# Kernel optimization log

Measured on AMD Instinct MI355X. Metric: run time of the kernel, lower is better.

Reference implementation:

```python
import jax, jax.numpy as jnp
import numpy as np

F, N, D, K = 32, 4096, 64, 512
COMMITMENT_COST = 0.25


def setup_inputs() -> dict:
    key = jax.random.key(0)
    k1, k2 = jax.random.split(key)
    inputs = jax.random.normal(k1, (F, N, D), dtype=jnp.float32)
    # GlorotUniform on weight shape [F, D, K]
    limit = float(np.sqrt(6.0 / (D + K)))
    w = jax.random.uniform(k2, (F, D, K), dtype=jnp.float32, minval=-limit, maxval=limit)
    return {"inputs": inputs, "w": w}


def reference(inputs, w):
    # inputs: [F, N, D], w: [F, D, K]
    distances = (
        jnp.sum(inputs ** 2, axis=2, keepdims=True)
        - 2.0 * jnp.einsum('fnd,fdk->fnk', inputs, w)
        + jnp.sum(w ** 2, axis=1, keepdims=True)
    )
    enc_idx = jnp.argmin(distances, axis=2)  # [F, N]
    w_t = jnp.swapaxes(w, 1, 2)  # [F, K, D]
    quantized = jnp.take_along_axis(w_t, enc_idx[:, :, None], axis=1)  # [F, N, D]
    e_latent_loss = jnp.mean((jax.lax.stop_gradient(quantized) - inputs) ** 2)
    q_latent_loss = jnp.mean((quantized - jax.lax.stop_gradient(inputs)) ** 2)
    loss = q_latent_loss + COMMITMENT_COST * e_latent_loss
    # straight-through estimator
    output = inputs + jax.lax.stop_gradient(quantized - inputs)
    return output, loss
```

## Files before the change

kernel.cpp:

```cpp
#include <hip/hip_runtime.h>
#include <math.h>

#define NF 32
#define NN 4096
#define ND 64
#define NK 512

#define LOSS_SCALE (1.25f / (float)(NF * NN * ND))
#define TAU 3e-4f

#define NPARTIAL (NF * NN * 4 / 256)

typedef short bf16x8 __attribute__((ext_vector_type(8)));
typedef float f32x4 __attribute__((ext_vector_type(4)));

static __device__ __forceinline__ unsigned short f2bf_rne(float f) {
    unsigned int u = __float_as_uint(f);
    u += 0x7FFFu + ((u >> 16) & 1u);
    return (unsigned short)(u >> 16);
}
static __device__ __forceinline__ float bf2f(unsigned short h) {
    return __uint_as_float(((unsigned int)h) << 16);
}

static __device__ __forceinline__ void gload_lds16(const void* g, void* l) {
    __builtin_amdgcn_global_load_lds(
        (const __attribute__((address_space(1))) unsigned int*)g,
        (__attribute__((address_space(3))) unsigned int*)l, 16, 0, 0);
}

__global__ __launch_bounds__(256)
void vq_prep_w(const float* __restrict__ w, float* __restrict__ wt,
               unsigned short* __restrict__ wh, unsigned short* __restrict__ wl,
               float* __restrict__ w2h) {
    const int gid = blockIdx.x * 256 + threadIdx.x;
    const int dc = gid & 7;
    const int k  = (gid >> 3) & (NK - 1);
    const int f  = gid >> 12;
    const float* __restrict__ wf = w + (size_t)f * ND * NK;
    const size_t rowo = ((size_t)f * NK + k) * ND + dc * 8;

    float v[8];
    unsigned short hh[8], ll[8];
    float s = 0.0f;
#pragma unroll
    for (int j = 0; j < 8; ++j) {
        v[j] = wf[(dc * 8 + j) * NK + k];
        s = fmaf(v[j], v[j], s);
        hh[j] = f2bf_rne(v[j]);
        ll[j] = f2bf_rne(v[j] - bf2f(hh[j]));
    }
    *(float4*)(wt + rowo)     = make_float4(v[0], v[1], v[2], v[3]);
    *(float4*)(wt + rowo + 4) = make_float4(v[4], v[5], v[6], v[7]);
    *(ushort4*)(wh + rowo)     = make_ushort4(hh[0], hh[1], hh[2], hh[3]);
    *(ushort4*)(wh + rowo + 4) = make_ushort4(hh[4], hh[5], hh[6], hh[7]);
    *(ushort4*)(wl + rowo)     = make_ushort4(ll[0], ll[1], ll[2], ll[3]);
    *(ushort4*)(wl + rowo + 4) = make_ushort4(ll[4], ll[5], ll[6], ll[7]);

    s += __shfl_xor(s, 1, 64);
    s += __shfl_xor(s, 2, 64);
    s += __shfl_xor(s, 4, 64);
    if (dc == 0) w2h[f * NK + k] = 0.5f * s;
}

__global__ __launch_bounds__(256, 4)
void vq_argmin(const float* __restrict__ x_in,
               const unsigned short* __restrict__ wh,
               const unsigned short* __restrict__ wl,
               const float* __restrict__ w2h,
               float* __restrict__ pm1,
               float* __restrict__ pm2,
               float* __restrict__ pkm) {
    const int b2   = blockIdx.x;
    const int h    = b2 & 1;
    const int b    = b2 >> 1;
    const int j    = b >> 3;
    const int f    = (b & 7) * 4 + (j & 3);
    const int xt   = j >> 2;
    const int tid  = threadIdx.x;
    const int wave = tid >> 6;
    const int lane = tid & 63;
    const int lc   = lane & 15;
    const int q    = lane >> 4;
    const int n0   = xt * 128 + wave * 32;

    __shared__ float w2s[256];
    __shared__ __align__(16) unsigned short bstage[2][4096];

    w2s[tid] = w2h[f * NK + h * 256 + tid];

    bf16x8 ah[2][2], al[2][2];
    const float* __restrict__ xbase = x_in + ((size_t)f * NN + n0 + lc) * ND;
#pragma unroll
    for (int mt = 0; mt < 2; ++mt) {
#pragma unroll
        for (int s = 0; s < 2; ++s) {
            const float* p = xbase + mt * 16 * ND + s * 32 + q * 8;
            float4 u0 = *(const float4*)(p);
            float4 u1 = *(const float4*)(p + 4);
            float xv[8] = {-u0.x, -u0.y, -u0.z, -u0.w, -u1.x, -u1.y, -u1.z, -u1.w};
            bf16x8 hh, ll;
#pragma unroll
            for (int jj = 0; jj < 8; ++jj) {
                unsigned short hb = f2bf_rne(xv[jj]);
                unsigned short lb = f2bf_rne(xv[jj] - bf2f(hb));
                hh[jj] = (short)hb;
                ll[jj] = (short)lb;
            }
            ah[mt][s] = hh;
            al[mt][s] = ll;
        }
    }

    const unsigned short* __restrict__ whf = wh + (size_t)f * NK * ND;
    const unsigned short* __restrict__ wlf = wl + (size_t)f * NK * ND;

    float m1[8], m2[8], kmin[8];
#pragma unroll
    for (int ri = 0; ri < 8; ++ri) { m1[ri] = INFINITY; m2[ri] = INFINITY; kmin[ri] = INFINITY; }

#define STAGE(st, pb) do {                                                  \
    _Pragma("unroll")                                                       \
    for (int rep = 0; rep < 2; ++rep) {                                     \
        const int c  = wave * 2 + rep;                                      \
        const int tl = c >> 2;                                              \
        const int sg = (c >> 1) & 1;                                        \
        const unsigned short* src = ((c & 1) ? wlf : whf) +                 \
            (size_t)((h * 8 + (st)) * 32 + tl * 16 + lc) * ND + q * 8 + sg * 32; \
        gload_lds16(src, &bstage[pb][c * 512]);                             \
    }                                                                       \
} while (0)

    STAGE(0, 0);

    for (int st = 0; st < 8; ++st) {
        __syncthreads();
        if (st < 7) STAGE(st + 1, (st + 1) & 1);
        const unsigned short* __restrict__ bb = &bstage[st & 1][0];

#pragma unroll
        for (int tl = 0; tl < 2; ++tl) {
            const int col = h * 256 + st * 32 + tl * 16 + lc;
            bf16x8 bh0 = *(const bf16x8*)(bb + (tl * 4 + 0) * 512 + lane * 8);
            bf16x8 bl0 = *(const bf16x8*)(bb + (tl * 4 + 1) * 512 + lane * 8);
            bf16x8 bh1 = *(const bf16x8*)(bb + (tl * 4 + 2) * 512 + lane * 8);
            bf16x8 bl1 = *(const bf16x8*)(bb + (tl * 4 + 3) * 512 + lane * 8);
            const float w2 = w2s[st * 32 + tl * 16 + lc];
#pragma unroll
            for (int mt = 0; mt < 2; ++mt) {
                f32x4 c = {w2, w2, w2, w2};
                c = __builtin_amdgcn_mfma_f32_16x16x32_bf16(ah[mt][0], bh0, c, 0, 0, 0);
                c = __builtin_amdgcn_mfma_f32_16x16x32_bf16(ah[mt][1], bh1, c, 0, 0, 0);
                c = __builtin_amdgcn_mfma_f32_16x16x32_bf16(ah[mt][0], bl0, c, 0, 0, 0);
                c = __builtin_amdgcn_mfma_f32_16x16x32_bf16(ah[mt][1], bl1, c, 0, 0, 0);
                c = __builtin_amdgcn_mfma_f32_16x16x32_bf16(al[mt][0], bh0, c, 0, 0, 0);
                c = __builtin_amdgcn_mfma_f32_16x16x32_bf16(al[mt][1], bh1, c, 0, 0, 0);
#pragma unroll
                for (int r = 0; r < 4; ++r) {
                    const int ri = mt * 4 + r;
                    const float sc = c[r];
                    const float key = __uint_as_float(
                        (__float_as_uint(sc) & 0xFFFFFE00u) | (unsigned int)col);
                    kmin[ri] = fminf(kmin[ri], key);
                    m2[ri] = __builtin_amdgcn_fmed3f(sc, m1[ri], m2[ri]);
                    m1[ri] = fminf(sc, m1[ri]);
                }
            }
        }
    }

#pragma unroll
    for (int ri = 0; ri < 8; ++ri) {
        float a1 = m1[ri], a2 = m2[ri], ak = kmin[ri];
#pragma unroll
        for (int off = 1; off < 16; off <<= 1) {
            const float b1 = __shfl_xor(a1, off, 64);
            const float b2 = __shfl_xor(a2, off, 64);
            const float bk = __shfl_xor(ak, off, 64);
            a2 = fminf(fminf(a2, b2), fmaxf(a1, b1));
            a1 = fminf(a1, b1);
            ak = fminf(ak, bk);
        }
        m1[ri] = a1; m2[ri] = a2; kmin[ri] = ak;
    }

    if (lc == 0) {
        const size_t FN = (size_t)NF * NN;
#pragma unroll
        for (int mt = 0; mt < 2; ++mt) {
            const int g = f * NN + n0 + mt * 16 + q * 4;
            float4 v1 = make_float4(m1[mt*4+0], m1[mt*4+1], m1[mt*4+2], m1[mt*4+3]);
            float4 v2 = make_float4(m2[mt*4+0], m2[mt*4+1], m2[mt*4+2], m2[mt*4+3]);
            float4 vk = make_float4(kmin[mt*4+0], kmin[mt*4+1], kmin[mt*4+2], kmin[mt*4+3]);
            *(float4*)(pm1 + h * FN + g) = v1;
            *(float4*)(pm2 + h * FN + g) = v2;
            *(float4*)(pkm + h * FN + g) = vk;
        }
    }
}

__global__ __launch_bounds__(256)
void vq_rescue(const float* __restrict__ x_in, const float* __restrict__ wt,
               const float* __restrict__ w2h,
               const float* __restrict__ pm1, const float* __restrict__ pm2,
               const float* __restrict__ pkm,
               unsigned int* __restrict__ keys) {
    const int lane = threadIdx.x & 63;
    const int wid  = (blockIdx.x * 256 + threadIdx.x) >> 6;
    const int base = wid * 16;
    const size_t FN = (size_t)NF * NN;

    int flag = 0;
    if (lane < 16) {
        const int g = base + lane;
        const float a1 = pm1[g], b1 = pm1[FN + g];
        const float a2 = pm2[g], b2 = pm2[FN + g];
        const float ka = pkm[g], kb = pkm[FN + g];
        const float m1f = fminf(a1, b1);
        const float m2f = fminf(fminf(a2, b2), fmaxf(a1, b1));
        const float kf  = fminf(ka, kb);
        keys[g] = __float_as_uint(kf) & 0x1FFu;
        flag = (m2f - m1f < TAU) ? 1 : 0;
    }
    unsigned long long m = __ballot(flag != 0);
    while (m) {
        const int r = __ffsll(m) - 1;
        m &= m - 1;
        const int g = base + r;
        const int f = g >> 12;
        const float* __restrict__ xr  = x_in + (size_t)g * ND;
        const float* __restrict__ wtf = wt + (size_t)f * NK * ND;
        unsigned long long best = 0xFFFFFFFFFFFFFFFFULL;
#pragma unroll 1
        for (int jj = 0; jj < 8; ++jj) {
            const int col = jj * 64 + lane;
            const float* __restrict__ wr = wtf + (size_t)col * ND;
            float t = w2h[f * NK + col];
#pragma unroll
            for (int d = 0; d < ND; d += 4) {
                float4 xv = *(const float4*)(xr + d);
                float4 wv = *(const float4*)(wr + d);
                t = fmaf(-xv.x, wv.x, t);
                t = fmaf(-xv.y, wv.y, t);
                t = fmaf(-xv.z, wv.z, t);
                t = fmaf(-xv.w, wv.w, t);
            }
            unsigned int u = __float_as_uint(t);
            u ^= (unsigned int)((int)u >> 31) | 0x80000000u;
            const unsigned long long key =
                ((unsigned long long)u << 32) | (unsigned int)col;
            best = key < best ? key : best;
        }
#pragma unroll
        for (int off = 32; off > 0; off >>= 1) {
            const unsigned long long o = __shfl_xor(best, off, 64);
            best = o < best ? o : best;
        }
        if (lane == 0) keys[g] = (unsigned int)(best & 0xFFFFFFFFULL);
    }
}

__global__ __launch_bounds__(256)
void vq_gather(const float* __restrict__ x_in, const float* __restrict__ wt,
               const unsigned int* __restrict__ keys, float* __restrict__ out,
               float* __restrict__ partial) {
    const int gid = blockIdx.x * 256 + threadIdx.x;
    const int row = gid >> 2;
    const int c   = (gid & 3) * 16;
    const int f   = row >> 12;
    const unsigned int k = keys[row];

    const float* __restrict__ q16 = wt + ((size_t)f * NK + k) * ND + c;
    const float* __restrict__ x16 = x_in + (size_t)row * ND + c;
    float* __restrict__ o16       = out + (size_t)row * ND + c;

    float lsum = 0.0f;
#pragma unroll
    for (int jj = 0; jj < 4; ++jj) {
        float4 qv = *(const float4*)(q16 + 4 * jj);
        float4 xv = *(const float4*)(x16 + 4 * jj);
        const float dx0 = qv.x - xv.x;
        const float dx1 = qv.y - xv.y;
        const float dx2 = qv.z - xv.z;
        const float dx3 = qv.w - xv.w;
        lsum = fmaf(dx0, dx0, lsum);
        lsum = fmaf(dx1, dx1, lsum);
        lsum = fmaf(dx2, dx2, lsum);
        lsum = fmaf(dx3, dx3, lsum);
        *(float4*)(o16 + 4 * jj) = qv;
    }

#pragma unroll
    for (int off = 32; off > 0; off >>= 1) {
        lsum += __shfl_down(lsum, off, 64);
    }
    __shared__ float wsum[4];
    if ((threadIdx.x & 63) == 0) wsum[threadIdx.x >> 6] = lsum;
    __syncthreads();
    if (threadIdx.x == 0) {
        partial[blockIdx.x] = wsum[0] + wsum[1] + wsum[2] + wsum[3];
    }
}

__global__ __launch_bounds__(256)
void vq_loss_final(const float* __restrict__ partial, float* __restrict__ loss) {
    float s = 0.0f;
    for (int i = threadIdx.x; i < NPARTIAL; i += 256) s += partial[i];
#pragma unroll
    for (int off = 32; off > 0; off >>= 1) s += __shfl_down(s, off, 64);
    __shared__ float wsum[4];
    if ((threadIdx.x & 63) == 0) wsum[threadIdx.x >> 6] = s;
    __syncthreads();
    if (threadIdx.x == 0) {
        *loss = (wsum[0] + wsum[1] + wsum[2] + wsum[3]) * LOSS_SCALE;
    }
}

extern "C" void kernel_launch(void* const* d_in, const int* in_sizes, int n_in,
                              void* d_out, int out_size, void* d_ws, size_t ws_size,
                              hipStream_t stream) {
    const float* x_in = (const float*)d_in[0];
    const float* w    = (const float*)d_in[1];
    float* out        = (float*)d_out;

    float* wt  = (float*)d_ws;
    float* w2h = wt + (size_t)NF * NK * ND;
    unsigned short* wh = (unsigned short*)(w2h + NF * NK);
    unsigned short* wl = wh + (size_t)NF * NK * ND;
    unsigned int* keys = (unsigned int*)(wl + (size_t)NF * NK * ND);
    float* pm1 = (float*)(keys + (size_t)NF * NN);
    float* pm2 = pm1 + (size_t)2 * NF * NN;
    float* pkm = pm2 + (size_t)2 * NF * NN;
    float* partial = pkm + (size_t)2 * NF * NN;

    float* loss_slot = out + (size_t)NF * NN * ND;

    vq_prep_w<<<NF * NK * 8 / 256, 256, 0, stream>>>(w, wt, wh, wl, w2h);

    vq_argmin<<<NF * NN / 64, 256, 0, stream>>>(x_in, wh, wl, w2h, pm1, pm2, pkm);

    vq_rescue<<<NF * NN / 16 / 4, 256, 0, stream>>>(x_in, wt, w2h, pm1, pm2, pkm, keys);

    vq_gather<<<NF * NN * 4 / 256, 256, 0, stream>>>(x_in, wt, keys, out, partial);

    vq_loss_final<<<1, 256, 0, stream>>>(partial, loss_slot);
}
```

Before: 165.8 us.

## Pre-pack codebook into MFMA fragment layout and load directly to registers

The weight-prep kernel now writes the hi/lo bf16 codebook into a fragment-ordered packed buffer, so each lane's MFMA B operand is one contiguous 16-byte chunk. The argmin kernel drops the LDS double-buffered staging and its per-stage barriers, and instead loads fragments straight from global memory into registers, prefetching the next tile. This removes LDS traffic and synchronisation, but every wave now reads the codebook from global/L2 separately instead of sharing it through LDS, and the prefetch adds register pressure.

```diff
diff --git a/kernel.cpp b/kernel.cpp
--- a/kernel.cpp
+++ b/kernel.cpp
@@ -23,16 +23,9 @@
     return __uint_as_float(((unsigned int)h) << 16);
 }
 
-static __device__ __forceinline__ void gload_lds16(const void* g, void* l) {
-    __builtin_amdgcn_global_load_lds(
-        (const __attribute__((address_space(1))) unsigned int*)g,
-        (__attribute__((address_space(3))) unsigned int*)l, 16, 0, 0);
-}
-
 __global__ __launch_bounds__(256)
 void vq_prep_w(const float* __restrict__ w, float* __restrict__ wt,
-               unsigned short* __restrict__ wh, unsigned short* __restrict__ wl,
-               float* __restrict__ w2h) {
+               unsigned short* __restrict__ wpk, float* __restrict__ w2h) {
     const int gid = blockIdx.x * 256 + threadIdx.x;
     const int dc = gid & 7;
     const int k  = (gid >> 3) & (NK - 1);
@@ -52,10 +45,18 @@
     }
     *(float4*)(wt + rowo)     = make_float4(v[0], v[1], v[2], v[3]);
     *(float4*)(wt + rowo + 4) = make_float4(v[4], v[5], v[6], v[7]);
-    *(ushort4*)(wh + rowo)     = make_ushort4(hh[0], hh[1], hh[2], hh[3]);
-    *(ushort4*)(wh + rowo + 4) = make_ushort4(hh[4], hh[5], hh[6], hh[7]);
-    *(ushort4*)(wl + rowo)     = make_ushort4(ll[0], ll[1], ll[2], ll[3]);
-    *(ushort4*)(wl + rowo + 4) = make_ushort4(ll[4], ll[5], ll[6], ll[7]);
+
+    const int lc  = k & 15;
+    const int ct  = k >> 4;
+    const int sdx = dc >> 2;
+    const int qq  = dc & 3;
+    const int ln  = qq * 16 + lc;
+    unsigned short* dsth = wpk + ((((size_t)f * 32 + ct) * 4 + sdx) * 64 + ln) * 8;
+    unsigned short* dstl = wpk + ((((size_t)f * 32 + ct) * 4 + 2 + sdx) * 64 + ln) * 8;
+    *(ushort4*)(dsth)     = make_ushort4(hh[0], hh[1], hh[2], hh[3]);
+    *(ushort4*)(dsth + 4) = make_ushort4(hh[4], hh[5], hh[6], hh[7]);
+    *(ushort4*)(dstl)     = make_ushort4(ll[0], ll[1], ll[2], ll[3]);
+    *(ushort4*)(dstl + 4) = make_ushort4(ll[4], ll[5], ll[6], ll[7]);
 
     s += __shfl_xor(s, 1, 64);
     s += __shfl_xor(s, 2, 64);
@@ -65,8 +66,7 @@
 
 __global__ __launch_bounds__(256, 4)
 void vq_argmin(const float* __restrict__ x_in,
-               const unsigned short* __restrict__ wh,
-               const unsigned short* __restrict__ wl,
+               const unsigned short* __restrict__ wpk,
                const float* __restrict__ w2h,
                float* __restrict__ pm1,
                float* __restrict__ pm2,
@@ -85,7 +85,6 @@
     const int n0   = xt * 128 + wave * 32;
 
     __shared__ float w2s[256];
-    __shared__ __align__(16) unsigned short bstage[2][4096];
 
     w2s[tid] = w2h[f * NK + h * 256 + tid];
 
@@ -112,61 +111,56 @@
         }
     }
 
-    const unsigned short* __restrict__ whf = wh + (size_t)f * NK * ND;
-    const unsigned short* __restrict__ wlf = wl + (size_t)f * NK * ND;
+    __syncthreads();
 
     float m1[8], m2[8], kmin[8];
 #pragma unroll
     for (int ri = 0; ri < 8; ++ri) { m1[ri] = INFINITY; m2[ri] = INFINITY; kmin[ri] = INFINITY; }
 
-#define STAGE(st, pb) do {                                                  \
-    _Pragma("unroll")                                                       \
-    for (int rep = 0; rep < 2; ++rep) {                                     \
-        const int c  = wave * 2 + rep;                                      \
-        const int tl = c >> 2;                                              \
-        const int sg = (c >> 1) & 1;                                        \
-        const unsigned short* src = ((c & 1) ? wlf : whf) +                 \
-            (size_t)((h * 8 + (st)) * 32 + tl * 16 + lc) * ND + q * 8 + sg * 32; \
-        gload_lds16(src, &bstage[pb][c * 512]);                             \
-    }                                                                       \
-} while (0)
-
-    STAGE(0, 0);
-
-    for (int st = 0; st < 8; ++st) {
-        __syncthreads();
-        if (st < 7) STAGE(st + 1, (st + 1) & 1);
-        const unsigned short* __restrict__ bb = &bstage[st & 1][0];
-
-#pragma unroll
-        for (int tl = 0; tl < 2; ++tl) {
-            const int col = h * 256 + st * 32 + tl * 16 + lc;
-            bf16x8 bh0 = *(const bf16x8*)(bb + (tl * 4 + 0) * 512 + lane * 8);
-            bf16x8 bl0 = *(const bf16x8*)(bb + (tl * 4 + 1) * 512 + lane * 8);
-            bf16x8 bh1 = *(const bf16x8*)(bb + (tl * 4 + 2) * 512 + lane * 8);
-            bf16x8 bl1 = *(const bf16x8*)(bb + (tl * 4 + 3) * 512 + lane * 8);
-            const float w2 = w2s[st * 32 + tl * 16 + lc];
-#pragma unroll
-            for (int mt = 0; mt < 2; ++mt) {
-                f32x4 c = {w2, w2, w2, w2};
-                c = __builtin_amdgcn_mfma_f32_16x16x32_bf16(ah[mt][0], bh0, c, 0, 0, 0);
-                c = __builtin_amdgcn_mfma_f32_16x16x32_bf16(ah[mt][1], bh1, c, 0, 0, 0);
-                c = __builtin_amdgcn_mfma_f32_16x16x32_bf16(ah[mt][0], bl0, c, 0, 0, 0);
-                c = __builtin_amdgcn_mfma_f32_16x16x32_bf16(ah[mt][1], bl1, c, 0, 0, 0);
-                c = __builtin_amdgcn_mfma_f32_16x16x32_bf16(al[mt][0], bh0, c, 0, 0, 0);
-                c = __builtin_amdgcn_mfma_f32_16x16x32_bf16(al[mt][1], bh1, c, 0, 0, 0);
-#pragma unroll
-                for (int r = 0; r < 4; ++r) {
-                    const int ri = mt * 4 + r;
-                    const float sc = c[r];
-                    const float key = __uint_as_float(
-                        (__float_as_uint(sc) & 0xFFFFFE00u) | (unsigned int)col);
-                    kmin[ri] = fminf(kmin[ri], key);
-                    m2[ri] = __builtin_amdgcn_fmed3f(sc, m1[ri], m2[ri]);
-                    m1[ri] = fminf(sc, m1[ri]);
-                }
+    const unsigned short* __restrict__ wf =
+        wpk + (size_t)f * (32 * 4 * 512) + (size_t)h * 16 * 2048 + lane * 8;
+
+    bf16x8 c0, c1, c2, c3;
+    {
+        const unsigned short* p = wf;
+        c0 = *(const bf16x8*)(p);
+        c1 = *(const bf16x8*)(p + 512);
+        c2 = *(const bf16x8*)(p + 1024);
+        c3 = *(const bf16x8*)(p + 1536);
+    }
+#pragma unroll
+    for (int ct2 = 0; ct2 < 16; ++ct2) {
+        bf16x8 n0, n1, n2, n3;
+        if (ct2 < 15) {
+            const unsigned short* p = wf + (size_t)(ct2 + 1) * 2048;
+            n0 = *(const bf16x8*)(p);
+            n1 = *(const bf16x8*)(p + 512);
+            n2 = *(const bf16x8*)(p + 1024);
+            n3 = *(const bf16x8*)(p + 1536);
+        }
+        const int col = h * 256 + ct2 * 16 + lc;
+        const float w2 = w2s[ct2 * 16 + lc];
+#pragma unroll
+        for (int mt = 0; mt < 2; ++mt) {
+            f32x4 c = {w2, w2, w2, w2};
+            c = __builtin_amdgcn_mfma_f32_16x16x32_bf16(ah[mt][0], c0, c, 0, 0, 0);
+            c = __builtin_amdgcn_mfma_f32_16x16x32_bf16(ah[mt][1], c1, c, 0, 0, 0);
+            c = __builtin_amdgcn_mfma_f32_16x16x32_bf16(ah[mt][0], c2, c, 0, 0, 0);
+            c = __builtin_amdgcn_mfma_f32_16x16x32_bf16(ah[mt][1], c3, c, 0, 0, 0);
+            c = __builtin_amdgcn_mfma_f32_16x16x32_bf16(al[mt][0], c0, c, 0, 0, 0);
+            c = __builtin_amdgcn_mfma_f32_16x16x32_bf16(al[mt][1], c1, c, 0, 0, 0);
+#pragma unroll
+            for (int r = 0; r < 4; ++r) {
+                const int ri = mt * 4 + r;
+                const float sc = c[r];
+                const float key = __uint_as_float(
+                    (__float_as_uint(sc) & 0xFFFFFE00u) | (unsigned int)col);
+                kmin[ri] = fminf(kmin[ri], key);
+                m2[ri] = __builtin_amdgcn_fmed3f(sc, m1[ri], m2[ri]);
+                m1[ri] = fminf(sc, m1[ri]);
             }
         }
+        c0 = n0; c1 = n1; c2 = n2; c3 = n3;
     }
 
 #pragma unroll
@@ -325,9 +319,8 @@
 
     float* wt  = (float*)d_ws;
     float* w2h = wt + (size_t)NF * NK * ND;
-    unsigned short* wh = (unsigned short*)(w2h + NF * NK);
-    unsigned short* wl = wh + (size_t)NF * NK * ND;
-    unsigned int* keys = (unsigned int*)(wl + (size_t)NF * NK * ND);
+    unsigned short* wpk = (unsigned short*)(w2h + NF * NK);
+    unsigned int* keys = (unsigned int*)(wpk + (size_t)2 * NF * NK * ND);
     float* pm1 = (float*)(keys + (size_t)NF * NN);
     float* pm2 = pm1 + (size_t)2 * NF * NN;
     float* pkm = pm2 + (size_t)2 * NF * NN;
@@ -335,9 +328,9 @@
 
     float* loss_slot = out + (size_t)NF * NN * ND;
 
-    vq_prep_w<<<NF * NK * 8 / 256, 256, 0, stream>>>(w, wt, wh, wl, w2h);
-
-    vq_argmin<<<NF * NN / 64, 256, 0, stream>>>(x_in, wh, wl, w2h, pm1, pm2, pkm);
+    vq_prep_w<<<NF * NK * 8 / 256, 256, 0, stream>>>(w, wt, wpk, w2h);
+
+    vq_argmin<<<NF * NN / 64, 256, 0, stream>>>(x_in, wpk, w2h, pm1, pm2, pkm);
 
     vq_rescue<<<NF * NN / 16 / 4, 256, 0, stream>>>(x_in, wt, w2h, pm1, pm2, pkm, keys);
 
```

After: 163.2 us. No clear change (-1.5%).

## Stage full codebook half in LDS once and loop over row tiles; tile weight transpose

Applied to the files above, without the earlier changes.

The argmin kernel now loads its whole half-codebook slice (8 stages, 64KB) into LDS up front and reuses it for two 128-row tiles per block. This replaces the per-block double-buffered streaming and halves the grid, cutting redundant codebook traffic and per-stage barriers. The cost is less overlap between load and compute, and occupancy drops to 2 blocks per CU because of the larger LDS footprint. The weight prep kernel now transposes through a padded LDS tile so that global reads are coalesced, with each thread handling 16 values.

```diff
diff --git a/kernel.cpp b/kernel.cpp
--- a/kernel.cpp
+++ b/kernel.cpp
@@ -33,37 +33,57 @@
 void vq_prep_w(const float* __restrict__ w, float* __restrict__ wt,
                unsigned short* __restrict__ wh, unsigned short* __restrict__ wl,
                float* __restrict__ w2h) {
-    const int gid = blockIdx.x * 256 + threadIdx.x;
-    const int dc = gid & 7;
-    const int k  = (gid >> 3) & (NK - 1);
-    const int f  = gid >> 12;
+    __shared__ float lds[64 * 65];
+    const int t  = threadIdx.x;
+    const int f  = blockIdx.x >> 3;
+    const int k0 = (blockIdx.x & 7) * 64;
     const float* __restrict__ wf = w + (size_t)f * ND * NK;
-    const size_t rowo = ((size_t)f * NK + k) * ND + dc * 8;
-
-    float v[8];
-    unsigned short hh[8], ll[8];
+
+    {
+        const int d = t >> 2, qq = t & 3;
+#pragma unroll
+        for (int i = 0; i < 4; ++i) {
+            const int c4 = qq + i * 4;
+            const float4 v = *(const float4*)(wf + (size_t)d * NK + k0 + c4 * 4);
+            lds[d * 65 + c4 * 4 + 0] = v.x;
+            lds[d * 65 + c4 * 4 + 1] = v.y;
+            lds[d * 65 + c4 * 4 + 2] = v.z;
+            lds[d * 65 + c4 * 4 + 3] = v.w;
+        }
+    }
+    __syncthreads();
+
+    const int k = t >> 2, p = t & 3;
+    float v[16];
     float s = 0.0f;
 #pragma unroll
-    for (int j = 0; j < 8; ++j) {
-        v[j] = wf[(dc * 8 + j) * NK + k];
+    for (int j = 0; j < 16; ++j) {
+        v[j] = lds[(p * 16 + j) * 65 + k];
         s = fmaf(v[j], v[j], s);
+    }
+    s += __shfl_xor(s, 1, 64);
+    s += __shfl_xor(s, 2, 64);
+    if (p == 0) w2h[f * NK + k0 + k] = 0.5f * s;
+
+    const size_t rowo = ((size_t)f * NK + k0 + k) * ND + p * 16;
+    unsigned short hh[16], ll[16];
+#pragma unroll
+    for (int j = 0; j < 16; ++j) {
         hh[j] = f2bf_rne(v[j]);
         ll[j] = f2bf_rne(v[j] - bf2f(hh[j]));
     }
-    *(float4*)(wt + rowo)     = make_float4(v[0], v[1], v[2], v[3]);
-    *(float4*)(wt + rowo + 4) = make_float4(v[4], v[5], v[6], v[7]);
-    *(ushort4*)(wh + rowo)     = make_ushort4(hh[0], hh[1], hh[2], hh[3]);
-    *(ushort4*)(wh + rowo + 4) = make_ushort4(hh[4], hh[5], hh[6], hh[7]);
-    *(ushort4*)(wl + rowo)     = make_ushort4(ll[0], ll[1], ll[2], ll[3]);
-    *(ushort4*)(wl + rowo + 4) = make_ushort4(ll[4], ll[5], ll[6], ll[7]);
-
-    s += __shfl_xor(s, 1, 64);
-    s += __shfl_xor(s, 2, 64);
-    s += __shfl_xor(s, 4, 64);
-    if (dc == 0) w2h[f * NK + k] = 0.5f * s;
-}
-
-__global__ __launch_bounds__(256, 4)
+#pragma unroll
+    for (int i = 0; i < 4; ++i) {
+        *(float4*)(wt + rowo + i * 4) =
+            make_float4(v[i*4+0], v[i*4+1], v[i*4+2], v[i*4+3]);
+        *(ushort4*)(wh + rowo + i * 4) =
+            make_ushort4(hh[i*4+0], hh[i*4+1], hh[i*4+2], hh[i*4+3]);
+        *(ushort4*)(wl + rowo + i * 4) =
+            make_ushort4(ll[i*4+0], ll[i*4+1], ll[i*4+2], ll[i*4+3]);
+    }
+}
+
+__global__ __launch_bounds__(256, 2)
 void vq_argmin(const float* __restrict__ x_in,
                const unsigned short* __restrict__ wh,
                const unsigned short* __restrict__ wl,
@@ -71,130 +91,133 @@
                float* __restrict__ pm1,
                float* __restrict__ pm2,
                float* __restrict__ pkm) {
-    const int b2   = blockIdx.x;
-    const int h    = b2 & 1;
-    const int b    = b2 >> 1;
-    const int j    = b >> 3;
-    const int f    = (b & 7) * 4 + (j & 3);
-    const int xt   = j >> 2;
+    const int b    = blockIdx.x;
+    const int fh   = b & 63;
+    const int f    = fh >> 1;
+    const int h    = fh & 1;
+    const int rg   = b >> 6;
     const int tid  = threadIdx.x;
     const int wave = tid >> 6;
     const int lane = tid & 63;
     const int lc   = lane & 15;
     const int q    = lane >> 4;
-    const int n0   = xt * 128 + wave * 32;
 
     __shared__ float w2s[256];
-    __shared__ __align__(16) unsigned short bstage[2][4096];
+    __shared__ __align__(16) unsigned short bstage[8][4096];
 
     w2s[tid] = w2h[f * NK + h * 256 + tid];
-
-    bf16x8 ah[2][2], al[2][2];
-    const float* __restrict__ xbase = x_in + ((size_t)f * NN + n0 + lc) * ND;
-#pragma unroll
-    for (int mt = 0; mt < 2; ++mt) {
-#pragma unroll
-        for (int s = 0; s < 2; ++s) {
-            const float* p = xbase + mt * 16 * ND + s * 32 + q * 8;
-            float4 u0 = *(const float4*)(p);
-            float4 u1 = *(const float4*)(p + 4);
-            float xv[8] = {-u0.x, -u0.y, -u0.z, -u0.w, -u1.x, -u1.y, -u1.z, -u1.w};
-            bf16x8 hh, ll;
-#pragma unroll
-            for (int jj = 0; jj < 8; ++jj) {
-                unsigned short hb = f2bf_rne(xv[jj]);
-                unsigned short lb = f2bf_rne(xv[jj] - bf2f(hb));
-                hh[jj] = (short)hb;
-                ll[jj] = (short)lb;
-            }
-            ah[mt][s] = hh;
-            al[mt][s] = ll;
-        }
-    }
 
     const unsigned short* __restrict__ whf = wh + (size_t)f * NK * ND;
     const unsigned short* __restrict__ wlf = wl + (size_t)f * NK * ND;
 
-    float m1[8], m2[8], kmin[8];
-#pragma unroll
-    for (int ri = 0; ri < 8; ++ri) { m1[ri] = INFINITY; m2[ri] = INFINITY; kmin[ri] = INFINITY; }
-
-#define STAGE(st, pb) do {                                                  \
-    _Pragma("unroll")                                                       \
-    for (int rep = 0; rep < 2; ++rep) {                                     \
-        const int c  = wave * 2 + rep;                                      \
-        const int tl = c >> 2;                                              \
-        const int sg = (c >> 1) & 1;                                        \
-        const unsigned short* src = ((c & 1) ? wlf : whf) +                 \
-            (size_t)((h * 8 + (st)) * 32 + tl * 16 + lc) * ND + q * 8 + sg * 32; \
-        gload_lds16(src, &bstage[pb][c * 512]);                             \
-    }                                                                       \
-} while (0)
-
-    STAGE(0, 0);
-
+#pragma unroll
     for (int st = 0; st < 8; ++st) {
-        __syncthreads();
-        if (st < 7) STAGE(st + 1, (st + 1) & 1);
-        const unsigned short* __restrict__ bb = &bstage[st & 1][0];
-
-#pragma unroll
-        for (int tl = 0; tl < 2; ++tl) {
-            const int col = h * 256 + st * 32 + tl * 16 + lc;
-            bf16x8 bh0 = *(const bf16x8*)(bb + (tl * 4 + 0) * 512 + lane * 8);
-            bf16x8 bl0 = *(const bf16x8*)(bb + (tl * 4 + 1) * 512 + lane * 8);
-            bf16x8 bh1 = *(const bf16x8*)(bb + (tl * 4 + 2) * 512 + lane * 8);
-            bf16x8 bl1 = *(const bf16x8*)(bb + (tl * 4 + 3) * 512 + lane * 8);
-            const float w2 = w2s[st * 32 + tl * 16 + lc];
+#pragma unroll
+        for (int rep = 0; rep < 2; ++rep) {
+            const int c  = wave * 2 + rep;
+            const int tl = c >> 2;
+            const int sg = (c >> 1) & 1;
+            const unsigned short* src = ((c & 1) ? wlf : whf) +
+                (size_t)((h * 8 + st) * 32 + tl * 16 + lc) * ND + q * 8 + sg * 32;
+            gload_lds16(src, &bstage[st][c * 512]);
+        }
+    }
+    __syncthreads();
+
+    for (int rt = 0; rt < 2; ++rt) {
+        const int n0 = rg * 256 + rt * 128 + wave * 32;
+
+        bf16x8 ah[2][2], al[2][2];
+        const float* __restrict__ xbase = x_in + ((size_t)f * NN + n0 + lc) * ND;
+#pragma unroll
+        for (int mt = 0; mt < 2; ++mt) {
+#pragma unroll
+            for (int s = 0; s < 2; ++s) {
+                const float* p = xbase + mt * 16 * ND + s * 32 + q * 8;
+                float4 u0 = *(const float4*)(p);
+                float4 u1 = *(const float4*)(p + 4);
+                float xv[8] = {-u0.x, -u0.y, -u0.z, -u0.w,
+                               -u1.x, -u1.y, -u1.z, -u1.w};
+                bf16x8 hh, ll;
+#pragma unroll
+                for (int jj = 0; jj < 8; ++jj) {
+                    unsigned short hb = f2bf_rne(xv[jj]);
+                    unsigned short lb = f2bf_rne(xv[jj] - bf2f(hb));
+                    hh[jj] = (short)hb;
+                    ll[jj] = (short)lb;
+                }
+                ah[mt][s] = hh;
+                al[mt][s] = ll;
+            }
+        }
+
+        float m1[8], m2[8], kmin[8];
+#pragma unroll
+        for (int ri = 0; ri < 8; ++ri) {
+            m1[ri] = INFINITY; m2[ri] = INFINITY; kmin[ri] = INFINITY;
+        }
+
+#pragma unroll
+        for (int st = 0; st < 8; ++st) {
+            const unsigned short* __restrict__ bb = &bstage[st][0];
+#pragma unroll
+            for (int tl = 0; tl < 2; ++tl) {
+                const int col = h * 256 + st * 32 + tl * 16 + lc;
+                bf16x8 bh0 = *(const bf16x8*)(bb + (tl * 4 + 0) * 512 + lane * 8);
+                bf16x8 bl0 = *(const bf16x8*)(bb + (tl * 4 + 1) * 512 + lane * 8);
+                bf16x8 bh1 = *(const bf16x8*)(bb + (tl * 4 + 2) * 512 + lane * 8);
+                bf16x8 bl1 = *(const bf16x8*)(bb + (tl * 4 + 3) * 512 + lane * 8);
+                const float w2 = w2s[st * 32 + tl * 16 + lc];
+#pragma unroll
+                for (int mt = 0; mt < 2; ++mt) {
+                    f32x4 c = {w2, w2, w2, w2};
+                    c = __builtin_amdgcn_mfma_f32_16x16x32_bf16(ah[mt][0], bh0, c, 0, 0, 0);
+                    c = __builtin_amdgcn_mfma_f32_16x16x32_bf16(ah[mt][1], bh1, c, 0, 0, 0);
+                    c = __builtin_amdgcn_mfma_f32_16x16x32_bf16(ah[mt][0], bl0, c, 0, 0, 0);
+                    c = __builtin_amdgcn_mfma_f32_16x16x32_bf16(ah[mt][1], bl1, c, 0, 0, 0);
+                    c = __builtin_amdgcn_mfma_f32_16x16x32_bf16(al[mt][0], bh0, c, 0, 0, 0);
+                    c = __builtin_amdgcn_mfma_f32_16x16x32_bf16(al[mt][1], bh1, c, 0, 0, 0);
+#pragma unroll
+                    for (int r = 0; r < 4; ++r) {
+                        const int ri = mt * 4 + r;
+                        const float sc = c[r];
+                        const float key = __uint_as_float(
+                            (__float_as_uint(sc) & 0xFFFFFE00u) | (unsigned int)col);
+                        kmin[ri] = fminf(kmin[ri], key);
+                        m2[ri] = __builtin_amdgcn_fmed3f(sc, m1[ri], m2[ri]);
+                        m1[ri] = fminf(sc, m1[ri]);
+                    }
+                }
+            }
+        }
+
+#pragma unroll
+        for (int ri = 0; ri < 8; ++ri) {
+            float a1 = m1[ri], a2 = m2[ri], ak = kmin[ri];
+#pragma unroll
+            for (int off = 1; off < 16; off <<= 1) {
+                const float b1 = __shfl_xor(a1, off, 64);
+                const float b2 = __shfl_xor(a2, off, 64);
+                const float bk = __shfl_xor(ak, off, 64);
+                a2 = fminf(fminf(a2, b2), fmaxf(a1, b1));
+                a1 = fminf(a1, b1);
+                ak = fminf(ak, bk);
+            }
+            m1[ri] = a1; m2[ri] = a2; kmin[ri] = ak;
+        }
+
+        if (lc == 0) {
+            const size_t FN = (size_t)NF * NN;
 #pragma unroll
             for (int mt = 0; mt < 2; ++mt) {
-                f32x4 c = {w2, w2, w2, w2};
-                c = __builtin_amdgcn_mfma_f32_16x16x32_bf16(ah[mt][0], bh0, c, 0, 0, 0);
-                c = __builtin_amdgcn_mfma_f32_16x16x32_bf16(ah[mt][1], bh1, c, 0, 0, 0);
-                c = __builtin_amdgcn_mfma_f32_16x16x32_bf16(ah[mt][0], bl0, c, 0, 0, 0);
-                c = __builtin_amdgcn_mfma_f32_16x16x32_bf16(ah[mt][1], bl1, c, 0, 0, 0);
-                c = __builtin_amdgcn_mfma_f32_16x16x32_bf16(al[mt][0], bh0, c, 0, 0, 0);
-                c = __builtin_amdgcn_mfma_f32_16x16x32_bf16(al[mt][1], bh1, c, 0, 0, 0);
-#pragma unroll
-                for (int r = 0; r < 4; ++r) {
-                    const int ri = mt * 4 + r;
-                    const float sc = c[r];
-                    const float key = __uint_as_float(
-                        (__float_as_uint(sc) & 0xFFFFFE00u) | (unsigned int)col);
-                    kmin[ri] = fminf(kmin[ri], key);
-                    m2[ri] = __builtin_amdgcn_fmed3f(sc, m1[ri], m2[ri]);
-                    m1[ri] = fminf(sc, m1[ri]);
-                }
-            }
-        }
-    }
-
-#pragma unroll
-    for (int ri = 0; ri < 8; ++ri) {
-        float a1 = m1[ri], a2 = m2[ri], ak = kmin[ri];
-#pragma unroll
-        for (int off = 1; off < 16; off <<= 1) {
-            const float b1 = __shfl_xor(a1, off, 64);
-            const float b2 = __shfl_xor(a2, off, 64);
-            const float bk = __shfl_xor(ak, off, 64);
-            a2 = fminf(fminf(a2, b2), fmaxf(a1, b1));
-            a1 = fminf(a1, b1);
-            ak = fminf(ak, bk);
-        }
-        m1[ri] = a1; m2[ri] = a2; kmin[ri] = ak;
-    }
-
-    if (lc == 0) {
-        const size_t FN = (size_t)NF * NN;
-#pragma unroll
-        for (int mt = 0; mt < 2; ++mt) {
-            const int g = f * NN + n0 + mt * 16 + q * 4;
-            float4 v1 = make_float4(m1[mt*4+0], m1[mt*4+1], m1[mt*4+2], m1[mt*4+3]);
-            float4 v2 = make_float4(m2[mt*4+0], m2[mt*4+1], m2[mt*4+2], m2[mt*4+3]);
-            float4 vk = make_float4(kmin[mt*4+0], kmin[mt*4+1], kmin[mt*4+2], kmin[mt*4+3]);
-            *(float4*)(pm1 + h * FN + g) = v1;
-            *(float4*)(pm2 + h * FN + g) = v2;
-            *(float4*)(pkm + h * FN + g) = vk;
+                const int g = f * NN + n0 + mt * 16 + q * 4;
+                float4 v1 = make_float4(m1[mt*4+0], m1[mt*4+1], m1[mt*4+2], m1[mt*4+3]);
+                float4 v2 = make_float4(m2[mt*4+0], m2[mt*4+1], m2[mt*4+2], m2[mt*4+3]);
+                float4 vk = make_float4(kmin[mt*4+0], kmin[mt*4+1], kmin[mt*4+2], kmin[mt*4+3]);
+                *(float4*)(pm1 + h * FN + g) = v1;
+                *(float4*)(pm2 + h * FN + g) = v2;
+                *(float4*)(pkm + h * FN + g) = vk;
+            }
         }
     }
 }
@@ -335,9 +358,9 @@
 
     float* loss_slot = out + (size_t)NF * NN * ND;
 
-    vq_prep_w<<<NF * NK * 8 / 256, 256, 0, stream>>>(w, wt, wh, wl, w2h);
-
-    vq_argmin<<<NF * NN / 64, 256, 0, stream>>>(x_in, wh, wl, w2h, pm1, pm2, pkm);
+    vq_prep_w<<<NF * 8, 256, 0, stream>>>(w, wt, wh, wl, w2h);
+
+    vq_argmin<<<NF * 2 * 16, 256, 0, stream>>>(x_in, wh, wl, w2h, pm1, pm2, pkm);
 
     vq_rescue<<<NF * NN / 16 / 4, 256, 0, stream>>>(x_in, wt, w2h, pm1, pm2, pkm, keys);
 
```

Result: slower. 253.2 us (+52.7%).
